# Optimization experiments

Hardware: AMD Instinct MI355X
Metric: run time of the kernel (lower is better)

Reference implementation:

```python
import jax, jax.numpy as jnp
import numpy as np

SINKHORN_ITERS = 5
EPS = 1e-12  # torch F.normalize eps


def _l2norm(x):
    n = jnp.sqrt(jnp.sum(x * x, axis=-1, keepdims=True))
    return x / jnp.maximum(n, EPS)


def setup_inputs() -> dict:
    key = jax.random.key(0)
    k1, k2, k3, k4 = jax.random.split(key, 4)
    B, Nd, Ns, D, Dm = 8, 2048, 2048, 1024, 256
    drone_nodes = jax.random.normal(k1, (B, Nd, D), dtype=jnp.float32)
    sat_nodes = jax.random.normal(k2, (B, Ns, D), dtype=jnp.float32)
    # match_proj parameters (nn.Linear(d_model, match_dim))
    lim = 1.0 / np.sqrt(D)
    W = jax.random.uniform(k3, (D, Dm), minval=-lim, maxval=lim, dtype=jnp.float32)
    b = jax.random.uniform(k4, (Dm,), minval=-lim, maxval=lim, dtype=jnp.float32)
    return {"drone_nodes": drone_nodes, "sat_nodes": sat_nodes, "W": W, "b": b}


def reference(drone_nodes, sat_nodes, W, b):
    # project + L2-normalize each node embedding
    d = _l2norm(drone_nodes @ W + b)   # [B, Nd, Dm]
    s = _l2norm(sat_nodes @ W + b)     # [B, Ns, Dm]
    M0 = jnp.einsum('bnd,bmd->bnm', d, s)  # [B, Nd, Ns] cosine similarities
    M = M0
    for _ in range(SINKHORN_ITERS):
        M = M - jax.nn.logsumexp(M, axis=2, keepdims=True)
        M = M - jax.nn.logsumexp(M, axis=1, keepdims=True)
    assignment = jnp.exp(M)
    denom = min(d.shape[1], s.shape[1])
    match_score = jnp.sum(assignment * M0, axis=(1, 2)) / denom  # [B]
    return (assignment, match_score)
```

## Files before the change

kernel.cpp:

```cpp
#include <hip/hip_runtime.h>
#include <math.h>

#define BATCH 8
#define NNODE 2048
#define DIN   1024
#define DM    256
#define ROWS_TOTAL (BATCH * NNODE)

#define LOG2E 1.4426950408889634f
#define Q127  0.011359803471566641f

typedef unsigned short u16;
typedef __attribute__((ext_vector_type(8))) short short8;
typedef __attribute__((ext_vector_type(4))) float f32x4;

__device__ __forceinline__ u16 f2b(float f) {
    union { float f; unsigned u; } v; v.f = f;
    unsigned r = v.u + 0x7fffu + ((v.u >> 16) & 1u);
    return (u16)(r >> 16);
}
__device__ __forceinline__ float b2f(u16 h) {
    union { unsigned u; float f; } v; v.u = ((unsigned)h) << 16; return v.f;
}
__device__ __forceinline__ float dqi(unsigned wd, int k) {
    return (float)((int)(wd << ((3 - k) * 8)) >> 24);
}

__global__ __launch_bounds__(256) void cvgm_prep_w(
    const float* __restrict__ W, u16* __restrict__ Wt)
{
    __shared__ float t[32][33];
    const int tx = threadIdx.x & 31, ty = threadIdx.x >> 5;
    const int k0 = blockIdx.x * 32, c0 = blockIdx.y * 32;
    #pragma unroll
    for (int r = 0; r < 4; ++r) {
        const int kl = ty * 4 + r;
        t[kl][tx] = W[(size_t)(k0 + kl) * DM + c0 + tx];
    }
    __syncthreads();
    #pragma unroll
    for (int r = 0; r < 4; ++r) {
        const int cl = ty * 4 + r;
        Wt[(size_t)(c0 + cl) * DIN + k0 + tx] = f2b(t[tx][cl]);
    }
}

__global__ __launch_bounds__(512) void cvgm_proj_mfma(
    const float* __restrict__ Xd, const float* __restrict__ Xs,
    const u16* __restrict__ Wt, const float* __restrict__ bias,
    u16* __restrict__ Pd, u16* __restrict__ Ps)
{
    __shared__ u16 As[64 * 64];
    __shared__ u16 Bs[256 * 64];
    __shared__ float rsum[4][64];

    const float* X = blockIdx.y ? Xs : Xd;
    u16* P = blockIdx.y ? Ps : Pd;

    const int tid = threadIdx.x;
    const int lane = tid & 63, wid = tid >> 6;
    const int wr = wid >> 2, wc = wid & 3;
    const int l15 = lane & 15, l4 = lane >> 4;
    const int row0 = blockIdx.x * 64;

    f32x4 acc[2][4];
    #pragma unroll
    for (int m = 0; m < 2; ++m)
        #pragma unroll
        for (int n = 0; n < 4; ++n) acc[m][n] = (f32x4){0.f, 0.f, 0.f, 0.f};

    const int arow = tid >> 3, ac = tid & 7;

    for (int k0 = 0; k0 < DIN; k0 += 64) {
        const float* src = X + (size_t)(row0 + arow) * DIN + k0 + ac * 8;
        const float4 x0 = *(const float4*)src;
        const float4 x1 = *(const float4*)(src + 4);
        short8 wb[4];
        #pragma unroll
        for (int it = 0; it < 4; ++it) {
            const int id = it * 512 + tid;
            const int col = id >> 3, cc = id & 7;
            wb[it] = *(const short8*)(Wt + (size_t)col * DIN + k0 + cc * 8);
        }
        __syncthreads();
        short8 ap;
        ap[0]=(short)f2b(x0.x); ap[1]=(short)f2b(x0.y); ap[2]=(short)f2b(x0.z); ap[3]=(short)f2b(x0.w);
        ap[4]=(short)f2b(x1.x); ap[5]=(short)f2b(x1.y); ap[6]=(short)f2b(x1.z); ap[7]=(short)f2b(x1.w);
        *(short8*)(As + (arow * 8 + (ac ^ (arow & 7))) * 8) = ap;
        #pragma unroll
        for (int it = 0; it < 4; ++it) {
            const int id = it * 512 + tid;
            const int col = id >> 3, cc = id & 7;
            *(short8*)(Bs + (col * 8 + (cc ^ (col & 7))) * 8) = wb[it];
        }
        __syncthreads();
        #pragma unroll
        for (int ks = 0; ks < 2; ++ks) {
            const int ch = ks * 4 + l4;
            short8 af[2], bfr[4];
            #pragma unroll
            for (int m = 0; m < 2; ++m) {
                const int row = wr * 32 + m * 16 + l15;
                af[m] = *(const short8*)(As + (row * 8 + (ch ^ (row & 7))) * 8);
            }
            #pragma unroll
            for (int n = 0; n < 4; ++n) {
                const int col = wc * 64 + n * 16 + l15;
                bfr[n] = *(const short8*)(Bs + (col * 8 + (ch ^ (col & 7))) * 8);
            }
            #pragma unroll
            for (int m = 0; m < 2; ++m)
                #pragma unroll
                for (int n = 0; n < 4; ++n)
                    acc[m][n] = __builtin_amdgcn_mfma_f32_16x16x32_bf16(af[m], bfr[n], acc[m][n], 0, 0, 0);
        }
        __syncthreads();
    }

    #pragma unroll
    for (int n = 0; n < 4; ++n) {
        const float bv = bias[wc * 64 + n * 16 + l15];
        #pragma unroll
        for (int m = 0; m < 2; ++m)
            #pragma unroll
            for (int r = 0; r < 4; ++r) acc[m][n][r] += bv;
    }
    #pragma unroll
    for (int m = 0; m < 2; ++m)
        #pragma unroll
        for (int r = 0; r < 4; ++r) {
            float s = 0.f;
            #pragma unroll
            for (int n = 0; n < 4; ++n) s += acc[m][n][r] * acc[m][n][r];
            s += __shfl_xor(s, 1); s += __shfl_xor(s, 2);
            s += __shfl_xor(s, 4); s += __shfl_xor(s, 8);
            if (l15 == 0) rsum[wc][wr * 32 + m * 16 + l4 * 4 + r] = s;
        }
    __syncthreads();
    #pragma unroll
    for (int m = 0; m < 2; ++m)
        #pragma unroll
        for (int r = 0; r < 4; ++r) {
            const int row = wr * 32 + m * 16 + l4 * 4 + r;
            const float tot = rsum[0][row] + rsum[1][row] + rsum[2][row] + rsum[3][row];
            const float inv = 1.0f / fmaxf(sqrtf(tot), 1e-12f);
            #pragma unroll
            for (int n = 0; n < 4; ++n) {
                const int col = wc * 64 + n * 16 + l15;
                P[(size_t)(row0 + row) * DM + col] = f2b(acc[m][n][r] * inv);
            }
        }
}

template <int WQ>
__global__ __launch_bounds__(256) void cvgm_m0_mfma(
    const u16* __restrict__ Dp, const u16* __restrict__ Sp,
    u16* __restrict__ C, char* __restrict__ Cq)
{
    __shared__ u16 As[128 * 64];
    __shared__ u16 Bs[128 * 64];

    const int tid = threadIdx.x;
    const int lane = tid & 63, wid = tid >> 6;
    const int wr = wid >> 1, wc = wid & 1;
    const int l15 = lane & 15, l4 = lane >> 4;
    const int bb = blockIdx.z;
    const int i0 = blockIdx.y * 128, j0 = blockIdx.x * 128;
    const u16* Db = Dp + (size_t)bb * NNODE * DM;
    const u16* Sb = Sp + (size_t)bb * NNODE * DM;

    f32x4 acc[4][4];
    #pragma unroll
    for (int m = 0; m < 4; ++m)
        #pragma unroll
        for (int n = 0; n < 4; ++n) acc[m][n] = (f32x4){0.f, 0.f, 0.f, 0.f};

    for (int k0 = 0; k0 < DM; k0 += 64) {
        short8 ra[4], rb[4];
        #pragma unroll
        for (int it = 0; it < 4; ++it) {
            const int id = it * 256 + tid;
            const int row = id >> 3, c = id & 7;
            ra[it] = *(const short8*)(Db + (size_t)(i0 + row) * DM + k0 + c * 8);
            rb[it] = *(const short8*)(Sb + (size_t)(j0 + row) * DM + k0 + c * 8);
        }
        __syncthreads();
        #pragma unroll
        for (int it = 0; it < 4; ++it) {
            const int id = it * 256 + tid;
            const int row = id >> 3, c = id & 7;
            const int sl = row * 8 + (c ^ (row & 7));
            *(short8*)(As + sl * 8) = ra[it];
            *(short8*)(Bs + sl * 8) = rb[it];
        }
        __syncthreads();
        #pragma unroll
        for (int ks = 0; ks < 2; ++ks) {
            const int ch = ks * 4 + l4;
            short8 af[4], bfr[4];
            #pragma unroll
            for (int m = 0; m < 4; ++m) {
                const int row = wr * 64 + m * 16 + l15;
                af[m] = *(const short8*)(As + (row * 8 + (ch ^ (row & 7))) * 8);
            }
            #pragma unroll
            for (int n = 0; n < 4; ++n) {
                const int col = wc * 64 + n * 16 + l15;
                bfr[n] = *(const short8*)(Bs + (col * 8 + (ch ^ (col & 7))) * 8);
            }
            #pragma unroll
            for (int m = 0; m < 4; ++m)
                #pragma unroll
                for (int n = 0; n < 4; ++n)
                    acc[m][n] = __builtin_amdgcn_mfma_f32_16x16x32_bf16(af[m], bfr[n], acc[m][n], 0, 0, 0);
        }
        __syncthreads();
    }

    u16* Cb = C + (size_t)bb * NNODE * NNODE;
    char* Cqb = Cq + (size_t)bb * NNODE * NNODE;
    #pragma unroll
    for (int m = 0; m < 4; ++m) {
        const int row = i0 + wr * 64 + m * 16 + l4 * 4;
        #pragma unroll
        for (int n = 0; n < 4; ++n) {
            const int col = j0 + wc * 64 + n * 16 + l15;
            #pragma unroll
            for (int r = 0; r < 4; ++r) {
                const float val = acc[m][n][r];
                Cb[(size_t)(row + r) * NNODE + col] = f2b(val);
                if constexpr (WQ) {
                    int q = __float2int_rn(val * 127.f);
                    q = q > 127 ? 127 : (q < -127 ? -127 : q);
                    Cqb[(size_t)(row + r) * NNODE + col] = (char)q;
                }
            }
        }
    }
}

template <int ISQ>
__global__ __launch_bounds__(256) void cvgm_rc(
    const void* __restrict__ Mq_, const float* __restrict__ v2,
    float* __restrict__ u2, float* __restrict__ ps)
{
    constexpr int RPC = ISQ ? 32 : 16;
    constexpr int NCH = NNODE / RPC;
    constexpr int RB  = ISQ ? NNODE : NNODE * 2;
    __shared__ alignas(16) char stripe[RPC * RB];
    __shared__ float u2s[RPC];

    const int tid = threadIdx.x;
    const int lane = tid & 63, w = tid >> 6;
    const int b = blockIdx.y, chunk = blockIdx.x;
    const size_t grow0 = ((size_t)b << 11) + chunk * RPC;

    float vl[32];
    const float* v2b = v2 + (b << 11);
    #pragma unroll
    for (int s = 0; s < 2; ++s)
        #pragma unroll
        for (int k = 0; k < 4; ++k)
            *(float4*)(vl + s * 16 + k * 4) =
                *(const float4*)(v2b + s * 1024 + lane * 16 + k * 4);

    const char* gbase = (const char*)Mq_ + grow0 * RB;
    constexpr int RW = RPC / 4;
    #pragma unroll
    for (int rr = 0; rr < RW; ++rr) {
        const int r = w * RW + rr;
        float s = 0.f;
        if constexpr (ISQ) {
            const char* rsrc = gbase + (size_t)r * RB;
            #pragma unroll
            for (int seg = 0; seg < 2; ++seg) {
                const int4 d = *(const int4*)(rsrc + seg * 1024 + lane * 16);
                *(int4*)(stripe + r * RB + seg * 1024 + lane * 16) = d;
                const unsigned uu[4] = {(unsigned)d.x, (unsigned)d.y, (unsigned)d.z, (unsigned)d.w};
                #pragma unroll
                for (int q = 0; q < 4; ++q)
                    #pragma unroll
                    for (int k = 0; k < 4; ++k)
                        s += exp2f(fmaf(dqi(uu[q], k), Q127, -vl[seg * 16 + q * 4 + k]));
            }
        } else {
            const char* rsrc = gbase + (size_t)r * RB;
            #pragma unroll
            for (int seg = 0; seg < 2; ++seg) {
                const int4 d0 = *(const int4*)(rsrc + seg * 2048 + lane * 32);
                const int4 d1 = *(const int4*)(rsrc + seg * 2048 + lane * 32 + 16);
                *(int4*)(stripe + r * RB + seg * 2048 + lane * 32) = d0;
                *(int4*)(stripe + r * RB + seg * 2048 + lane * 32 + 16) = d1;
                const unsigned uu[8] = {(unsigned)d0.x, (unsigned)d0.y, (unsigned)d0.z, (unsigned)d0.w,
                                        (unsigned)d1.x, (unsigned)d1.y, (unsigned)d1.z, (unsigned)d1.w};
                #pragma unroll
                for (int q = 0; q < 8; ++q) {
                    union { unsigned u; float f; } lo, hi;
                    lo.u = uu[q] << 16; hi.u = uu[q] & 0xffff0000u;
                    s += exp2f(fmaf(lo.f, LOG2E, -vl[seg * 16 + q * 2 + 0]));
                    s += exp2f(fmaf(hi.f, LOG2E, -vl[seg * 16 + q * 2 + 1]));
                }
            }
        }
        #pragma unroll
        for (int off = 1; off < 64; off <<= 1) s += __shfl_xor(s, off);
        if (lane == 0) {
            const float l2 = __log2f(s);
            u2[grow0 + r] = l2;
            u2s[r] = l2;
        }
    }
    __syncthreads();

    const int j = tid * 8;
    float sc[8] = {0.f, 0.f, 0.f, 0.f, 0.f, 0.f, 0.f, 0.f};
    #pragma unroll 4
    for (int i = 0; i < RPC; ++i) {
        const float ui = u2s[i];
        if constexpr (ISQ) {
            const unsigned* pw = (const unsigned*)(stripe + i * RB + j);
            const unsigned w0 = pw[0], w1 = pw[1];
            #pragma unroll
            for (int k = 0; k < 4; ++k) {
                sc[k]     += exp2f(fmaf(dqi(w0, k), Q127, -ui));
                sc[4 + k] += exp2f(fmaf(dqi(w1, k), Q127, -ui));
            }
        } else {
            const unsigned* pw = (const unsigned*)(stripe + i * RB + j * 2);
            #pragma unroll
            for (int q = 0; q < 4; ++q) {
                union { unsigned u; float f; } lo, hi;
                lo.u = pw[q] << 16; hi.u = pw[q] & 0xffff0000u;
                sc[q * 2 + 0] += exp2f(fmaf(lo.f, LOG2E, -ui));
                sc[q * 2 + 1] += exp2f(fmaf(hi.f, LOG2E, -ui));
            }
        }
    }
    float* dst = ps + ((size_t)(b * NCH + chunk)) * NNODE + j;
    *(float4*)(dst)     = make_float4(sc[0], sc[1], sc[2], sc[3]);
    *(float4*)(dst + 4) = make_float4(sc[4], sc[5], sc[6], sc[7]);
}

__global__ __launch_bounds__(256) void cvgm_merge(
    const float* __restrict__ ps, float* __restrict__ v2, int nch)
{
    const int idx = blockIdx.x * 256 + threadIdx.x;
    const int b = idx >> 11, j = idx & 2047;
    float s = 0.f;
    #pragma unroll 8
    for (int c = 0; c < nch; ++c) s += ps[(size_t)(b * nch + c) * NNODE + j];
    v2[idx] = __log2f(s);
}

__global__ __launch_bounds__(256) void cvgm_final(
    const u16* __restrict__ M0b, const float* __restrict__ u2,
    const float* __restrict__ v2, float* __restrict__ out,
    float* __restrict__ spart)
{
    const int tid = threadIdx.x;
    const int lane = tid & 63, w = tid >> 6;
    const int b = blockIdx.y, chunk = blockIdx.x;
    const size_t grow0 = ((size_t)b << 11) + chunk * 32;

    float vl[32];
    const float* v2b = v2 + (b << 11);
    #pragma unroll
    for (int s = 0; s < 2; ++s)
        #pragma unroll
        for (int k = 0; k < 4; ++k)
            *(float4*)(vl + s * 16 + k * 4) =
                *(const float4*)(v2b + s * 1024 + lane * 16 + k * 4);

    #pragma unroll
    for (int rr = 0; rr < 8; ++rr) {
        const size_t grow = grow0 + w * 8 + rr;
        const float ui = u2[grow];
        const char* rsrc = (const char*)(M0b + grow * NNODE);
        float* drow = out + grow * NNODE;
        float acc = 0.f;
        #pragma unroll
        for (int seg = 0; seg < 2; ++seg) {
            const int4 d0 = *(const int4*)(rsrc + seg * 2048 + lane * 32);
            const int4 d1 = *(const int4*)(rsrc + seg * 2048 + lane * 32 + 16);
            const unsigned uu[8] = {(unsigned)d0.x, (unsigned)d0.y, (unsigned)d0.z, (unsigned)d0.w,
                                    (unsigned)d1.x, (unsigned)d1.y, (unsigned)d1.z, (unsigned)d1.w};
            float a[16];
            #pragma unroll
            for (int q = 0; q < 8; ++q) {
                union { unsigned u; float f; } lo, hi;
                lo.u = uu[q] << 16; hi.u = uu[q] & 0xffff0000u;
                const float e0 = exp2f(fmaf(lo.f, LOG2E, -(ui + vl[seg * 16 + q * 2 + 0])));
                const float e1 = exp2f(fmaf(hi.f, LOG2E, -(ui + vl[seg * 16 + q * 2 + 1])));
                a[q * 2 + 0] = e0; a[q * 2 + 1] = e1;
                acc += e0 * lo.f + e1 * hi.f;
            }
            float* dseg = drow + seg * 1024 + lane * 16;
            #pragma unroll
            for (int k = 0; k < 4; ++k)
                *(float4*)(dseg + k * 4) = make_float4(a[k*4+0], a[k*4+1], a[k*4+2], a[k*4+3]);
        }
        #pragma unroll
        for (int off = 1; off < 64; off <<= 1) acc += __shfl_xor(acc, off);
        if (lane == 0) spart[grow] = acc;
    }
}

__global__ __launch_bounds__(256) void cvgm_score(
    const float* __restrict__ spart, float* __restrict__ score)
{
    const int b = blockIdx.x;
    float acc = 0.f;
    for (int t = threadIdx.x; t < NNODE; t += 256) acc += spart[(b << 11) + t];
    #pragma unroll
    for (int off = 1; off < 64; off <<= 1) acc += __shfl_xor(acc, off);
    __shared__ float sh[4];
    if ((threadIdx.x & 63) == 0) sh[threadIdx.x >> 6] = acc;
    __syncthreads();
    if (threadIdx.x == 0) score[b] = (sh[0] + sh[1] + sh[2] + sh[3]) * (1.0f / 2048.0f);
}

extern "C" void kernel_launch(void* const* d_in, const int* in_sizes, int n_in,
                              void* d_out, int out_size, void* d_ws, size_t ws_size,
                              hipStream_t stream) {
    (void)in_sizes; (void)n_in; (void)out_size;
    const float* drone = (const float*)d_in[0];
    const float* sat   = (const float*)d_in[1];
    const float* W     = (const float*)d_in[2];
    const float* bias  = (const float*)d_in[3];

    float* out   = (float*)d_out;
    float* score = out + (size_t)BATCH * NNODE * NNODE;

    char* ws = (char*)d_ws;
    const size_t SZ_M0B  = (size_t)BATCH * NNODE * NNODE * 2;
    const size_t SZ_M0Q  = (size_t)BATCH * NNODE * NNODE;
    const size_t SZ_PROJ = (size_t)ROWS_TOTAL * DM * 2;
    const size_t SZ_WT   = (size_t)DM * DIN * 2;
    const size_t SZ_UV   = (size_t)ROWS_TOTAL * 4;
    const size_t SZ_PS   = (size_t)BATCH * 128 * NNODE * 4;

    const size_t NEED_I8  = SZ_M0B + SZ_M0Q + 2 * SZ_PROJ + SZ_WT + 3 * SZ_UV + SZ_PS;
    const bool use_i8 = ws_size >= NEED_I8;

    size_t off = 0;
    u16* M0b = (u16*)(ws + off); off += SZ_M0B;
    char* M0q = (char*)(ws + off); if (use_i8) off += SZ_M0Q;
    u16* dproj = (u16*)(ws + off); off += SZ_PROJ;
    u16* sproj = (u16*)(ws + off); off += SZ_PROJ;
    u16* Wt = (u16*)(ws + off); off += SZ_WT;
    float* u2 = (float*)(ws + off); off += SZ_UV;
    float* v2 = (float*)(ws + off); off += SZ_UV;
    float* ps = (float*)(ws + off); off += SZ_PS;
    float* spart = (float*)(ws + off);

    hipMemsetAsync(v2, 0, SZ_UV, stream);
    cvgm_prep_w<<<dim3(32, 8), 256, 0, stream>>>(W, Wt);
    cvgm_proj_mfma<<<dim3(256, 2), 512, 0, stream>>>(drone, sat, Wt, bias, dproj, sproj);

    if (use_i8) {
        cvgm_m0_mfma<1><<<dim3(16, 16, 8), 256, 0, stream>>>(dproj, sproj, M0b, M0q);
        for (int it = 0; it < 5; ++it) {
            cvgm_rc<1><<<dim3(64, 8), 256, 0, stream>>>(M0q, v2, u2, ps);
            cvgm_merge<<<ROWS_TOTAL / 256, 256, 0, stream>>>(ps, v2, 64);
        }
    } else {
        cvgm_m0_mfma<0><<<dim3(16, 16, 8), 256, 0, stream>>>(dproj, sproj, M0b, M0q);
        for (int it = 0; it < 5; ++it) {
            cvgm_rc<0><<<dim3(128, 8), 256, 0, stream>>>(M0b, v2, u2, ps);
            cvgm_merge<<<ROWS_TOTAL / 256, 256, 0, stream>>>(ps, v2, 128);
        }
    }

    cvgm_final<<<dim3(64, 8), 256, 0, stream>>>(M0b, u2, v2, out, spart);
    cvgm_score<<<BATCH, 256, 0, stream>>>(spart, score);
}
```

Measured before the change: 285.4 us.

## Use int8 similarity matrix everywhere with factored exp and register column sums

Drops the bf16 copy of M0 and runs every Sinkhorn pass and the final output from the int8-quantized matrix. The row/column passes now compute each exp(M0) once per element, scale it by precomputed exp(-v) for row sums, and accumulate column partials in registers instead of re-reading a shared stripe and recomputing exps. The final kernel is restructured to one row per block and reads int8 data, cutting memory traffic. The risks are quantization error in the final assignment output and score, and more partial-sum chunks to merge.

```diff
diff --git a/kernel.cpp b/kernel.cpp
--- a/kernel.cpp
+++ b/kernel.cpp
@@ -9,6 +9,7 @@
 
 #define LOG2E 1.4426950408889634f
 #define Q127  0.011359803471566641f
+#define INV127 0.007874015748031496f
 
 typedef unsigned short u16;
 typedef __attribute__((ext_vector_type(8))) short short8;
@@ -18,9 +19,6 @@
     union { float f; unsigned u; } v; v.f = f;
     unsigned r = v.u + 0x7fffu + ((v.u >> 16) & 1u);
     return (u16)(r >> 16);
-}
-__device__ __forceinline__ float b2f(u16 h) {
-    union { unsigned u; float f; } v; v.u = ((unsigned)h) << 16; return v.f;
 }
 __device__ __forceinline__ float dqi(unsigned wd, int k) {
     return (float)((int)(wd << ((3 - k) * 8)) >> 24);
@@ -152,10 +150,9 @@
         }
 }
 
-template <int WQ>
 __global__ __launch_bounds__(256) void cvgm_m0_mfma(
     const u16* __restrict__ Dp, const u16* __restrict__ Sp,
-    u16* __restrict__ C, char* __restrict__ Cq)
+    char* __restrict__ Cq)
 {
     __shared__ u16 As[128 * 64];
     __shared__ u16 Bs[128 * 64];
@@ -217,7 +214,6 @@
         __syncthreads();
     }
 
-    u16* Cb = C + (size_t)bb * NNODE * NNODE;
     char* Cqb = Cq + (size_t)bb * NNODE * NNODE;
     #pragma unroll
     for (int m = 0; m < 4; ++m) {
@@ -227,182 +223,142 @@
             const int col = j0 + wc * 64 + n * 16 + l15;
             #pragma unroll
             for (int r = 0; r < 4; ++r) {
-                const float val = acc[m][n][r];
-                Cb[(size_t)(row + r) * NNODE + col] = f2b(val);
-                if constexpr (WQ) {
-                    int q = __float2int_rn(val * 127.f);
-                    q = q > 127 ? 127 : (q < -127 ? -127 : q);
-                    Cqb[(size_t)(row + r) * NNODE + col] = (char)q;
-                }
-            }
-        }
-    }
-}
-
-template <int ISQ>
+                int q = __float2int_rn(acc[m][n][r] * 127.f);
+                q = q > 127 ? 127 : (q < -127 ? -127 : q);
+                Cqb[(size_t)(row + r) * NNODE + col] = (char)q;
+            }
+        }
+    }
+}
+
 __global__ __launch_bounds__(256) void cvgm_rc(
-    const void* __restrict__ Mq_, const float* __restrict__ v2,
+    const char* __restrict__ Mq, const float* __restrict__ v2,
     float* __restrict__ u2, float* __restrict__ ps)
 {
-    constexpr int RPC = ISQ ? 32 : 16;
-    constexpr int NCH = NNODE / RPC;
-    constexpr int RB  = ISQ ? NNODE : NNODE * 2;
-    __shared__ alignas(16) char stripe[RPC * RB];
-    __shared__ float u2s[RPC];
+    __shared__ float cps[4][NNODE];
 
     const int tid = threadIdx.x;
     const int lane = tid & 63, w = tid >> 6;
     const int b = blockIdx.y, chunk = blockIdx.x;
-    const size_t grow0 = ((size_t)b << 11) + chunk * RPC;
-
-    float vl[32];
+    const size_t row0 = ((size_t)b << 11) + chunk * 16;
     const float* v2b = v2 + (b << 11);
+
+    float wv[32];
     #pragma unroll
     for (int s = 0; s < 2; ++s)
         #pragma unroll
+        for (int k = 0; k < 4; ++k) {
+            const float4 vv = *(const float4*)(v2b + s * 1024 + lane * 16 + k * 4);
+            wv[s*16+k*4+0] = exp2f(-vv.x);
+            wv[s*16+k*4+1] = exp2f(-vv.y);
+            wv[s*16+k*4+2] = exp2f(-vv.z);
+            wv[s*16+k*4+3] = exp2f(-vv.w);
+        }
+
+    const char* gb = Mq + row0 * NNODE + lane * 16;
+
+    float sc[32];
+    #pragma unroll
+    for (int k = 0; k < 32; ++k) sc[k] = 0.f;
+
+    #pragma unroll
+    for (int rr = 0; rr < 4; ++rr) {
+        const char* rsrc = gb + (size_t)(w * 4 + rr) * NNODE;
+        const int4 d0 = *(const int4*)(rsrc);
+        const int4 d1 = *(const int4*)(rsrc + 1024);
+        const unsigned qd[8] = {(unsigned)d0.x, (unsigned)d0.y, (unsigned)d0.z, (unsigned)d0.w,
+                                (unsigned)d1.x, (unsigned)d1.y, (unsigned)d1.z, (unsigned)d1.w};
+        float p[32];
+        #pragma unroll
+        for (int q = 0; q < 8; ++q)
+            #pragma unroll
+            for (int k = 0; k < 4; ++k)
+                p[q * 4 + k] = exp2f(dqi(qd[q], k) * Q127);
+        float s = 0.f;
+        #pragma unroll
+        for (int k = 0; k < 32; ++k) s = fmaf(p[k], wv[k], s);
+        #pragma unroll
+        for (int off = 1; off < 64; off <<= 1) s += __shfl_xor(s, off);
+        const float ur = __log2f(s);
+        if (lane == 0) u2[row0 + w * 4 + rr] = ur;
+        const float eu = exp2f(-ur);
+        #pragma unroll
+        for (int k = 0; k < 32; ++k) sc[k] = fmaf(p[k], eu, sc[k]);
+    }
+
+    #pragma unroll
+    for (int s = 0; s < 2; ++s)
+        #pragma unroll
         for (int k = 0; k < 4; ++k)
-            *(float4*)(vl + s * 16 + k * 4) =
-                *(const float4*)(v2b + s * 1024 + lane * 16 + k * 4);
-
-    const char* gbase = (const char*)Mq_ + grow0 * RB;
-    constexpr int RW = RPC / 4;
-    #pragma unroll
-    for (int rr = 0; rr < RW; ++rr) {
-        const int r = w * RW + rr;
-        float s = 0.f;
-        if constexpr (ISQ) {
-            const char* rsrc = gbase + (size_t)r * RB;
-            #pragma unroll
-            for (int seg = 0; seg < 2; ++seg) {
-                const int4 d = *(const int4*)(rsrc + seg * 1024 + lane * 16);
-                *(int4*)(stripe + r * RB + seg * 1024 + lane * 16) = d;
-                const unsigned uu[4] = {(unsigned)d.x, (unsigned)d.y, (unsigned)d.z, (unsigned)d.w};
-                #pragma unroll
-                for (int q = 0; q < 4; ++q)
-                    #pragma unroll
-                    for (int k = 0; k < 4; ++k)
-                        s += exp2f(fmaf(dqi(uu[q], k), Q127, -vl[seg * 16 + q * 4 + k]));
-            }
-        } else {
-            const char* rsrc = gbase + (size_t)r * RB;
-            #pragma unroll
-            for (int seg = 0; seg < 2; ++seg) {
-                const int4 d0 = *(const int4*)(rsrc + seg * 2048 + lane * 32);
-                const int4 d1 = *(const int4*)(rsrc + seg * 2048 + lane * 32 + 16);
-                *(int4*)(stripe + r * RB + seg * 2048 + lane * 32) = d0;
-                *(int4*)(stripe + r * RB + seg * 2048 + lane * 32 + 16) = d1;
-                const unsigned uu[8] = {(unsigned)d0.x, (unsigned)d0.y, (unsigned)d0.z, (unsigned)d0.w,
-                                        (unsigned)d1.x, (unsigned)d1.y, (unsigned)d1.z, (unsigned)d1.w};
-                #pragma unroll
-                for (int q = 0; q < 8; ++q) {
-                    union { unsigned u; float f; } lo, hi;
-                    lo.u = uu[q] << 16; hi.u = uu[q] & 0xffff0000u;
-                    s += exp2f(fmaf(lo.f, LOG2E, -vl[seg * 16 + q * 2 + 0]));
-                    s += exp2f(fmaf(hi.f, LOG2E, -vl[seg * 16 + q * 2 + 1]));
-                }
-            }
-        }
-        #pragma unroll
-        for (int off = 1; off < 64; off <<= 1) s += __shfl_xor(s, off);
-        if (lane == 0) {
-            const float l2 = __log2f(s);
-            u2[grow0 + r] = l2;
-            u2s[r] = l2;
-        }
-    }
+            *(float4*)(&cps[w][s * 1024 + lane * 16 + k * 4]) =
+                make_float4(sc[s*16+k*4+0], sc[s*16+k*4+1], sc[s*16+k*4+2], sc[s*16+k*4+3]);
     __syncthreads();
 
     const int j = tid * 8;
-    float sc[8] = {0.f, 0.f, 0.f, 0.f, 0.f, 0.f, 0.f, 0.f};
-    #pragma unroll 4
-    for (int i = 0; i < RPC; ++i) {
-        const float ui = u2s[i];
-        if constexpr (ISQ) {
-            const unsigned* pw = (const unsigned*)(stripe + i * RB + j);
-            const unsigned w0 = pw[0], w1 = pw[1];
-            #pragma unroll
-            for (int k = 0; k < 4; ++k) {
-                sc[k]     += exp2f(fmaf(dqi(w0, k), Q127, -ui));
-                sc[4 + k] += exp2f(fmaf(dqi(w1, k), Q127, -ui));
-            }
-        } else {
-            const unsigned* pw = (const unsigned*)(stripe + i * RB + j * 2);
-            #pragma unroll
-            for (int q = 0; q < 4; ++q) {
-                union { unsigned u; float f; } lo, hi;
-                lo.u = pw[q] << 16; hi.u = pw[q] & 0xffff0000u;
-                sc[q * 2 + 0] += exp2f(fmaf(lo.f, LOG2E, -ui));
-                sc[q * 2 + 1] += exp2f(fmaf(hi.f, LOG2E, -ui));
-            }
-        }
-    }
-    float* dst = ps + ((size_t)(b * NCH + chunk)) * NNODE + j;
-    *(float4*)(dst)     = make_float4(sc[0], sc[1], sc[2], sc[3]);
-    *(float4*)(dst + 4) = make_float4(sc[4], sc[5], sc[6], sc[7]);
+    float4 a0 = *(const float4*)(&cps[0][j]), a1 = *(const float4*)(&cps[0][j + 4]);
+    #pragma unroll
+    for (int ww = 1; ww < 4; ++ww) {
+        const float4 b0 = *(const float4*)(&cps[ww][j]);
+        const float4 b1 = *(const float4*)(&cps[ww][j + 4]);
+        a0.x += b0.x; a0.y += b0.y; a0.z += b0.z; a0.w += b0.w;
+        a1.x += b1.x; a1.y += b1.y; a1.z += b1.z; a1.w += b1.w;
+    }
+    float* dst = ps + ((size_t)(b * 128 + chunk)) * NNODE + j;
+    *(float4*)dst = a0;
+    *(float4*)(dst + 4) = a1;
 }
 
 __global__ __launch_bounds__(256) void cvgm_merge(
-    const float* __restrict__ ps, float* __restrict__ v2, int nch)
+    const float* __restrict__ ps, float* __restrict__ v2)
 {
     const int idx = blockIdx.x * 256 + threadIdx.x;
     const int b = idx >> 11, j = idx & 2047;
     float s = 0.f;
     #pragma unroll 8
-    for (int c = 0; c < nch; ++c) s += ps[(size_t)(b * nch + c) * NNODE + j];
+    for (int c = 0; c < 128; ++c) s += ps[(size_t)(b * 128 + c) * NNODE + j];
     v2[idx] = __log2f(s);
 }
 
-__global__ __launch_bounds__(256) void cvgm_final(
-    const u16* __restrict__ M0b, const float* __restrict__ u2,
+__global__ __launch_bounds__(128) void cvgm_final(
+    const char* __restrict__ Mq, const float* __restrict__ u2,
     const float* __restrict__ v2, float* __restrict__ out,
     float* __restrict__ spart)
 {
-    const int tid = threadIdx.x;
-    const int lane = tid & 63, w = tid >> 6;
-    const int b = blockIdx.y, chunk = blockIdx.x;
-    const size_t grow0 = ((size_t)b << 11) + chunk * 32;
-
-    float vl[32];
-    const float* v2b = v2 + (b << 11);
-    #pragma unroll
-    for (int s = 0; s < 2; ++s)
-        #pragma unroll
-        for (int k = 0; k < 4; ++k)
-            *(float4*)(vl + s * 16 + k * 4) =
-                *(const float4*)(v2b + s * 1024 + lane * 16 + k * 4);
-
-    #pragma unroll
-    for (int rr = 0; rr < 8; ++rr) {
-        const size_t grow = grow0 + w * 8 + rr;
-        const float ui = u2[grow];
-        const char* rsrc = (const char*)(M0b + grow * NNODE);
-        float* drow = out + grow * NNODE;
-        float acc = 0.f;
-        #pragma unroll
-        for (int seg = 0; seg < 2; ++seg) {
-            const int4 d0 = *(const int4*)(rsrc + seg * 2048 + lane * 32);
-            const int4 d1 = *(const int4*)(rsrc + seg * 2048 + lane * 32 + 16);
-            const unsigned uu[8] = {(unsigned)d0.x, (unsigned)d0.y, (unsigned)d0.z, (unsigned)d0.w,
-                                    (unsigned)d1.x, (unsigned)d1.y, (unsigned)d1.z, (unsigned)d1.w};
-            float a[16];
-            #pragma unroll
-            for (int q = 0; q < 8; ++q) {
-                union { unsigned u; float f; } lo, hi;
-                lo.u = uu[q] << 16; hi.u = uu[q] & 0xffff0000u;
-                const float e0 = exp2f(fmaf(lo.f, LOG2E, -(ui + vl[seg * 16 + q * 2 + 0])));
-                const float e1 = exp2f(fmaf(hi.f, LOG2E, -(ui + vl[seg * 16 + q * 2 + 1])));
-                a[q * 2 + 0] = e0; a[q * 2 + 1] = e1;
-                acc += e0 * lo.f + e1 * hi.f;
-            }
-            float* dseg = drow + seg * 1024 + lane * 16;
-            #pragma unroll
-            for (int k = 0; k < 4; ++k)
-                *(float4*)(dseg + k * 4) = make_float4(a[k*4+0], a[k*4+1], a[k*4+2], a[k*4+3]);
-        }
-        #pragma unroll
-        for (int off = 1; off < 64; off <<= 1) acc += __shfl_xor(acc, off);
-        if (lane == 0) spart[grow] = acc;
-    }
+    const int row = (blockIdx.y << 11) + blockIdx.x;
+    const int t = threadIdx.x;
+    const float ui = u2[row];
+    const float* v2b = v2 + (blockIdx.y << 11);
+
+    float vl[16];
+    #pragma unroll
+    for (int k = 0; k < 4; ++k)
+        *(float4*)(vl + k * 4) = *(const float4*)(v2b + t * 16 + k * 4);
+
+    const int4 d = *(const int4*)(Mq + (size_t)row * NNODE + t * 16);
+    const unsigned qd[4] = {(unsigned)d.x, (unsigned)d.y, (unsigned)d.z, (unsigned)d.w};
+
+    float a[16], acc = 0.f;
+    #pragma unroll
+    for (int q = 0; q < 4; ++q)
+        #pragma unroll
+        for (int k = 0; k < 4; ++k) {
+            const float xq = dqi(qd[q], k);
+            const float e = exp2f(fmaf(xq, Q127, -(ui + vl[q * 4 + k])));
+            a[q * 4 + k] = e;
+            acc = fmaf(e, xq, acc);
+        }
+    float* drow = out + (size_t)row * NNODE + t * 16;
+    #pragma unroll
+    for (int k = 0; k < 4; ++k)
+        *(float4*)(drow + k * 4) = make_float4(a[k*4+0], a[k*4+1], a[k*4+2], a[k*4+3]);
+
+    acc *= INV127;
+    #pragma unroll
+    for (int off = 1; off < 64; off <<= 1) acc += __shfl_xor(acc, off);
+    __shared__ float sh[2];
+    if ((t & 63) == 0) sh[t >> 6] = acc;
+    __syncthreads();
+    if (t == 0) spart[row] = sh[0] + sh[1];
 }
 
 __global__ __launch_bounds__(256) void cvgm_score(
@@ -422,7 +378,7 @@
 extern "C" void kernel_launch(void* const* d_in, const int* in_sizes, int n_in,
                               void* d_out, int out_size, void* d_ws, size_t ws_size,
                               hipStream_t stream) {
-    (void)in_sizes; (void)n_in; (void)out_size;
+    (void)in_sizes; (void)n_in; (void)out_size; (void)ws_size;
     const float* drone = (const float*)d_in[0];
     const float* sat   = (const float*)d_in[1];
     const float* W     = (const float*)d_in[2];
@@ -432,45 +388,32 @@
     float* score = out + (size_t)BATCH * NNODE * NNODE;
 
     char* ws = (char*)d_ws;
-    const size_t SZ_M0B  = (size_t)BATCH * NNODE * NNODE * 2;
     const size_t SZ_M0Q  = (size_t)BATCH * NNODE * NNODE;
     const size_t SZ_PROJ = (size_t)ROWS_TOTAL * DM * 2;
     const size_t SZ_WT   = (size_t)DM * DIN * 2;
     const size_t SZ_UV   = (size_t)ROWS_TOTAL * 4;
     const size_t SZ_PS   = (size_t)BATCH * 128 * NNODE * 4;
 
-    const size_t NEED_I8  = SZ_M0B + SZ_M0Q + 2 * SZ_PROJ + SZ_WT + 3 * SZ_UV + SZ_PS;
-    const bool use_i8 = ws_size >= NEED_I8;
-
     size_t off = 0;
-    u16* M0b = (u16*)(ws + off); off += SZ_M0B;
-    char* M0q = (char*)(ws + off); if (use_i8) off += SZ_M0Q;
-    u16* dproj = (u16*)(ws + off); off += SZ_PROJ;
-    u16* sproj = (u16*)(ws + off); off += SZ_PROJ;
-    u16* Wt = (u16*)(ws + off); off += SZ_WT;
-    float* u2 = (float*)(ws + off); off += SZ_UV;
-    float* v2 = (float*)(ws + off); off += SZ_UV;
-    float* ps = (float*)(ws + off); off += SZ_PS;
+    char* M0q  = ws + off;            off += SZ_M0Q;
+    u16* dproj = (u16*)(ws + off);    off += SZ_PROJ;
+    u16* sproj = (u16*)(ws + off);    off += SZ_PROJ;
+    u16* Wt    = (u16*)(ws + off);    off += SZ_WT;
+    float* u2  = (float*)(ws + off);  off += SZ_UV;
+    float* v2  = (float*)(ws + off);  off += SZ_UV;
+    float* ps  = (float*)(ws + off);  off += SZ_PS;
     float* spart = (float*)(ws + off);
 
     hipMemsetAsync(v2, 0, SZ_UV, stream);
     cvgm_prep_w<<<dim3(32, 8), 256, 0, stream>>>(W, Wt);
     cvgm_proj_mfma<<<dim3(256, 2), 512, 0, stream>>>(drone, sat, Wt, bias, dproj, sproj);
-
-    if (use_i8) {
-        cvgm_m0_mfma<1><<<dim3(16, 16, 8), 256, 0, stream>>>(dproj, sproj, M0b, M0q);
-        for (int it = 0; it < 5; ++it) {
-            cvgm_rc<1><<<dim3(64, 8), 256, 0, stream>>>(M0q, v2, u2, ps);
-            cvgm_merge<<<ROWS_TOTAL / 256, 256, 0, stream>>>(ps, v2, 64);
-        }
-    } else {
-        cvgm_m0_mfma<0><<<dim3(16, 16, 8), 256, 0, stream>>>(dproj, sproj, M0b, M0q);
-        for (int it = 0; it < 5; ++it) {
-            cvgm_rc<0><<<dim3(128, 8), 256, 0, stream>>>(M0b, v2, u2, ps);
-            cvgm_merge<<<ROWS_TOTAL / 256, 256, 0, stream>>>(ps, v2, 128);
-        }
-    }
-
-    cvgm_final<<<dim3(64, 8), 256, 0, stream>>>(M0b, u2, v2, out, spart);
+    cvgm_m0_mfma<<<dim3(16, 16, 8), 256, 0, stream>>>(dproj, sproj, M0q);
+
+    for (int it = 0; it < 5; ++it) {
+        cvgm_rc<<<dim3(128, 8), 256, 0, stream>>>(M0q, v2, u2, ps);
+        cvgm_merge<<<ROWS_TOTAL / 256, 256, 0, stream>>>(ps, v2);
+    }
+
+    cvgm_final<<<dim3(2048, 8), 128, 0, stream>>>(M0q, u2, v2, out, spart);
     cvgm_score<<<BATCH, 256, 0, stream>>>(spart, score);
 }
```

Result: faster. 262.7 us (-8.0%).
